# Optimization experiments

Measured on AMD Instinct MI355X. Metric: run time of the kernel, lower is better.

Reference implementation:

```python
import jax, jax.numpy as jnp
import numpy as np

B, S, D, H = 2, 2048, 1024, 16
DK = D // H


def setup_inputs() -> dict:
    key = jax.random.key(0)
    ks = jax.random.split(key, 12)
    scale = 1.0 / np.sqrt(D)
    inp = {
        "pre_Q": jax.random.normal(ks[0], (B, S, D), jnp.float32),
        "pre_K": jax.random.normal(ks[1], (B, S, D), jnp.float32),
        "pre_V": jax.random.normal(ks[2], (B, S, D), jnp.float32),
        "Wq": jax.random.normal(ks[3], (D, D), jnp.float32) * scale,
        "bq": jnp.zeros((D,), jnp.float32),
        "Wk": jax.random.normal(ks[4], (D, D), jnp.float32) * scale,
        "bk": jnp.zeros((D,), jnp.float32),
        "Wv": jax.random.normal(ks[5], (D, D), jnp.float32) * scale,
        "bv": jnp.zeros((D,), jnp.float32),
        "Wo": jax.random.normal(ks[6], (D, D), jnp.float32) * scale,
        "bo": jnp.zeros((D,), jnp.float32),
        "mask": jnp.ones((B, 1, 1, S), jnp.int32),
    }
    return inp


def _split_heads(x):
    # (B, S, D) -> (B, H, S, DK)
    return x.reshape(B, S, H, DK).transpose(0, 2, 1, 3)


def reference(pre_Q, pre_K, pre_V, Wq, bq, Wk, bk, Wv, bv, Wo, bo, mask):
    # linear projections (torch nn.Linear: x @ W.T + b)
    Q = _split_heads(pre_Q @ Wq.T + bq)
    K = _split_heads(pre_K @ Wk.T + bk)
    V = _split_heads(pre_V @ Wv.T + bv)
    # scaled dot-product attention; dropout is identity in eval mode
    scores = jnp.einsum("bhqd,bhkd->bhqk", Q, K) / np.sqrt(DK).astype(np.float32)
    scores = jnp.where(mask == 0, jnp.float32(-1e9), scores)
    weights = jax.nn.softmax(scores, axis=-1)
    ctx = jnp.einsum("bhqk,bhkd->bhqd", weights, V)  # (B, H, S, DK)
    concat = ctx.transpose(0, 2, 1, 3).reshape(B, S, D)
    return concat @ Wo.T + bo
```

## Files before the change

### kernel.cpp

```cpp
#include <hip/hip_runtime.h>

#define SS 2048
#define DD 1024
#define HH 16
#define MM 4096
#define KK 1024

typedef __attribute__((ext_vector_type(8))) short bf16x8;
typedef __attribute__((ext_vector_type(4))) float f32x4;
typedef __attribute__((ext_vector_type(4))) float float4_t;
typedef __attribute__((ext_vector_type(4))) short short4_t;
typedef __attribute__((ext_vector_type(4))) int iv4;

__device__ __forceinline__ short f2bf(float f) {
    union { float f; unsigned u; } x; x.f = f;
    unsigned r = x.u + 0x7fffu + ((x.u >> 16) & 1u);
    return (short)(r >> 16);
}

__device__ __forceinline__ f32x4 mfma16(bf16x8 a, bf16x8 b, f32x4 c) {
    return __builtin_amdgcn_mfma_f32_16x16x32_bf16(a, b, c, 0, 0, 0);
}

__device__ __forceinline__ void gl_lds16(const void* g, void* l) {
    __builtin_amdgcn_global_load_lds(
        (const __attribute__((address_space(1))) void*)g,
        (__attribute__((address_space(3))) void*)l, 16, 0, 0);
}

__global__ __launch_bounds__(256)
void convX(const float* __restrict__ x0, const float* __restrict__ x1,
           const float* __restrict__ x2, short* __restrict__ dst) {
    const float* s = (blockIdx.y == 0) ? x0 : (blockIdx.y == 1) ? x1 : x2;
    const size_t i = ((size_t)blockIdx.x * 256 + threadIdx.x) * 8;
    float4_t a = *(const float4_t*)(s + i);
    float4_t b = *(const float4_t*)(s + i + 4);
    bf16x8 o;
#pragma unroll
    for (int e = 0; e < 4; ++e) { o[e] = f2bf(a[e]); o[4 + e] = f2bf(b[e]); }
    *(bf16x8*)(dst + (size_t)blockIdx.y * MM * KK + i) = o;
}

__global__ __launch_bounds__(256)
void convW(const float* __restrict__ w0, const float* __restrict__ w1,
           const float* __restrict__ w2, const float* __restrict__ w3,
           short* __restrict__ dst) {
    const float* s = (blockIdx.y == 0) ? w0 : (blockIdx.y == 1) ? w1
                   : (blockIdx.y == 2) ? w2 : w3;
    const size_t i = ((size_t)blockIdx.x * 256 + threadIdx.x) * 8;
    float4_t a = *(const float4_t*)(s + i);
    float4_t b = *(const float4_t*)(s + i + 4);
    bf16x8 o;
#pragma unroll
    for (int e = 0; e < 4; ++e) { o[e] = f2bf(a[e]); o[4 + e] = f2bf(b[e]); }
    *(bf16x8*)(dst + (size_t)blockIdx.y * KK * KK + i) = o;
}

__device__ __forceinline__ void gemm_loop(const short* __restrict__ A,
                                          const short* __restrict__ Bw,
                                          int m0, int n0,
                                          short* As, short* Bs,
                                          f32x4 acc[4][4]) {
    const int tid = threadIdx.x;
    const int lane = tid & 63, w = tid >> 6;
    const int wr = w >> 1, wc = w & 1;
    const int lr = lane & 15, lg = lane >> 4;

    const int c1 = tid + 256;
    const int r0 = tid >> 2, o0 = (tid & 3) * 8;
    const int r1 = c1 >> 2, o1 = (c1 & 3) * 8;
    const short* ga0 = A + (size_t)(m0 + r0) * KK + o0;
    const short* ga1 = A + (size_t)(m0 + r1) * KK + o1;
    const short* gb0 = Bw + (size_t)(n0 + r0) * KK + o0;
    const short* gb1 = Bw + (size_t)(n0 + r1) * KK + o1;
    char* lA = (char*)As + tid * 16;
    char* lB = (char*)Bs + tid * 16;

#define GSTAGE(buf, kofs)                                  \
    { gl_lds16(ga0 + (kofs), lA + (buf) * 8192);           \
      gl_lds16(ga1 + (kofs), lA + 4096 + (buf) * 8192);    \
      gl_lds16(gb0 + (kofs), lB + (buf) * 8192);           \
      gl_lds16(gb1 + (kofs), lB + 4096 + (buf) * 8192); }

    GSTAGE(0, 0);
    __syncthreads();
    int cur = 0;
    for (int kt = 0; kt < KK / 32; ++kt) {
        if (kt + 1 < KK / 32) GSTAGE(cur ^ 1, (kt + 1) * 32);
        const char* ba = (const char*)As + cur * 8192;
        const char* bb = (const char*)Bs + cur * 8192;
        bf16x8 af[4], bfr[4];
#pragma unroll
        for (int i = 0; i < 4; ++i) {
            af[i]  = *(const bf16x8*)(ba + (wr * 64 + i * 16 + lr) * 64 + lg * 16);
            bfr[i] = *(const bf16x8*)(bb + (wc * 64 + i * 16 + lr) * 64 + lg * 16);
        }
#pragma unroll
        for (int mi = 0; mi < 4; ++mi)
#pragma unroll
            for (int ni = 0; ni < 4; ++ni)
                acc[mi][ni] = mfma16(af[mi], bfr[ni], acc[mi][ni]);
        __syncthreads();
        cur ^= 1;
    }
#undef GSTAGE
}

__global__ __launch_bounds__(256, 2)
void qkv_gemm(const short* __restrict__ Xb, const short* __restrict__ Wb,
              const float* __restrict__ bq, const float* __restrict__ bk,
              const float* __restrict__ bv,
              short* __restrict__ Qo, short* __restrict__ Ko, short* __restrict__ Vto) {
    __shared__ __align__(16) short As[2 * 4096];
    __shared__ __align__(16) short Bs[2 * 4096];
    const int z = blockIdx.z;
    const short* A = Xb + (size_t)z * MM * KK;
    const short* W = Wb + (size_t)z * KK * KK;
    const float* bias = (z == 0) ? bq : (z == 1) ? bk : bv;
    const float scale = (z == 0) ? 0.125f : 1.0f;
    const int m0 = blockIdx.x * 128, n0 = blockIdx.y * 128;

    f32x4 zero = {0.f, 0.f, 0.f, 0.f};
    f32x4 acc[4][4];
#pragma unroll
    for (int i = 0; i < 4; ++i)
#pragma unroll
        for (int j = 0; j < 4; ++j) acc[i][j] = zero;

    gemm_loop(A, W, m0, n0, As, Bs, acc);

    const int tid = threadIdx.x;
    const int lane = tid & 63, w = tid >> 6;
    const int wr = w >> 1, wc = w & 1;
    const int lr = lane & 15, lg = lane >> 4;

#pragma unroll
    for (int mi = 0; mi < 4; ++mi) {
        const int mbase = m0 + wr * 64 + mi * 16 + lg * 4;
        const int b = mbase >> 11, s = mbase & 2047;
#pragma unroll
        for (int ni = 0; ni < 4; ++ni) {
            const int n = n0 + wc * 64 + ni * 16 + lr;
            const float bvv = bias[n];
            const int h = n >> 6, dk = n & 63;
            if (z == 2) {
                short4_t pk;
#pragma unroll
                for (int r = 0; r < 4; ++r) pk[r] = f2bf(acc[mi][ni][r] + bvv);
                const int sp = (s & ~31) | (lg * 8 + (mi & 1) * 4);
                *(short4_t*)(Vto + ((size_t)((b * HH + h) * 64 + dk) << 11) + sp) = pk;
            } else {
                short* dst = (z == 0) ? Qo : Ko;
#pragma unroll
                for (int r = 0; r < 4; ++r)
                    dst[((size_t)((b * HH + h) * SS + (s + r)) << 6) + dk] =
                        f2bf((acc[mi][ni][r] + bvv) * scale);
            }
        }
    }
}

__global__ __launch_bounds__(256, 2)
void out_gemm(const short* __restrict__ ctx, const short* __restrict__ Wo,
              const float* __restrict__ bo, float* __restrict__ out) {
    __shared__ __align__(16) short As[2 * 4096];
    __shared__ __align__(16) short Bs[2 * 4096];
    const int m0 = blockIdx.x * 128, n0 = blockIdx.y * 128;

    f32x4 zero = {0.f, 0.f, 0.f, 0.f};
    f32x4 acc[4][4];
#pragma unroll
    for (int i = 0; i < 4; ++i)
#pragma unroll
        for (int j = 0; j < 4; ++j) acc[i][j] = zero;

    gemm_loop(ctx, Wo, m0, n0, As, Bs, acc);

    const int tid = threadIdx.x;
    const int lane = tid & 63, w = tid >> 6;
    const int wr = w >> 1, wc = w & 1;
    const int lr = lane & 15, lg = lane >> 4;

#pragma unroll
    for (int mi = 0; mi < 4; ++mi)
#pragma unroll
        for (int ni = 0; ni < 4; ++ni) {
            const int n = n0 + wc * 64 + ni * 16 + lr;
            const float bvv = bo[n];
#pragma unroll
            for (int r = 0; r < 4; ++r) {
                const int m = m0 + wr * 64 + mi * 16 + lg * 4 + r;
                out[(size_t)m * KK + n] = acc[mi][ni][r] + bvv;
            }
        }
}

__global__ __launch_bounds__(256, 2)
void attn_kernel(const short* __restrict__ Qg, const short* __restrict__ Kg,
                 const short* __restrict__ Vtg, const int* __restrict__ mask,
                 short* __restrict__ ctxb) {
    __shared__ __align__(16) short Ks[2][4096];
    __shared__ __align__(16) short Vs[2][4096];

    const int tid = threadIdx.x, w = tid >> 6, lane = tid & 63;
    const int lr = lane & 15, lg = lane >> 4;
    const int bh = blockIdx.y, b = bh >> 4, h = bh & 15;
    const int q0w = blockIdx.x * 64 + w * 16;

    const short* Qh = Qg + (size_t)bh * SS * 64;
    const short* Kh = Kg + (size_t)bh * SS * 64;
    const short* Vh = Vtg + (size_t)bh * 64 * SS;
    const int* mrow = mask + b * SS;

    bf16x8 qf0 = *(const bf16x8*)(Qh + (q0w + lr) * 64 + lg * 8);
    bf16x8 qf1 = *(const bf16x8*)(Qh + (q0w + lr) * 64 + 32 + lg * 8);

    f32x4 zero = {0.f, 0.f, 0.f, 0.f};
    f32x4 octx[4];
#pragma unroll
    for (int dt = 0; dt < 4; ++dt) octx[dt] = zero;
    float mrun = -1e30f, lrun = 0.f;

    const int c1 = tid + 256;
    const int kr0 = tid >> 3, kc0 = ((tid & 7) ^ (kr0 & 7)) * 8;
    const int kr1 = c1 >> 3, kc1 = ((c1 & 7) ^ (kr1 & 7)) * 8;
    const short* gk0 = Kh + kr0 * 64 + kc0;
    const short* gk1 = Kh + kr1 * 64 + kc1;
    const short* gv0 = Vh + (size_t)kr0 * SS + kc0;
    const short* gv1 = Vh + (size_t)kr1 * SS + kc1;
    char* lK = (char*)Ks + tid * 16;
    char* lV = (char*)Vs + tid * 16;

#define ASTAGE(buf, key0)                                    \
    { gl_lds16(gk0 + (key0) * 64, lK + (buf) * 8192);        \
      gl_lds16(gk1 + (key0) * 64, lK + 4096 + (buf) * 8192); \
      gl_lds16(gv0 + (key0), lV + (buf) * 8192);             \
      gl_lds16(gv1 + (key0), lV + 4096 + (buf) * 8192); }

    ASTAGE(0, 0);
    __syncthreads();
    int cur = 0;

    for (int it = 0; it < SS / 64; ++it) {
        const int key0 = it * 64;
        if (it + 1 < SS / 64) ASTAGE(cur ^ 1, key0 + 64);

        const char* bK = (const char*)Ks + cur * 8192;
        const char* bV = (const char*)Vs + cur * 8192;

        f32x4 sc[4];
#pragma unroll
        for (int kb = 0; kb < 4; ++kb) {
            const int row = kb * 16 + lr;
            const char* rb = bK + row * 128;
            const int sw = row & 7;
            bf16x8 k0 = *(const bf16x8*)(rb + ((lg ^ sw) * 16));
            bf16x8 k1 = *(const bf16x8*)(rb + (((4 + lg) ^ sw) * 16));
            f32x4 s = zero;
            s = mfma16(k0, qf0, s);
            s = mfma16(k1, qf1, s);
            sc[kb] = s;
        }
#pragma unroll
        for (int kb = 0; kb < 4; ++kb) {
            iv4 mv = *(const iv4*)(mrow + key0 + kb * 16 + lg * 4);
#pragma unroll
            for (int r = 0; r < 4; ++r)
                if (mv[r] == 0) sc[kb][r] = -1e9f;
        }
        float tm = -1e30f;
#pragma unroll
        for (int kb = 0; kb < 4; ++kb)
#pragma unroll
            for (int r = 0; r < 4; ++r) tm = fmaxf(tm, sc[kb][r]);
        tm = fmaxf(tm, __shfl_xor(tm, 16));
        tm = fmaxf(tm, __shfl_xor(tm, 32));
        const float mnew = fmaxf(mrun, tm);
        float rs = 0.f;
#pragma unroll
        for (int kb = 0; kb < 4; ++kb)
#pragma unroll
            for (int r = 0; r < 4; ++r) {
                const float p = __expf(sc[kb][r] - mnew);
                sc[kb][r] = p;
                rs += p;
            }
        rs += __shfl_xor(rs, 16);
        rs += __shfl_xor(rs, 32);
        const float alpha = __expf(mrun - mnew);
        lrun = lrun * alpha + rs;
        mrun = mnew;

        float aq[4];
#pragma unroll
        for (int r = 0; r < 4; ++r) aq[r] = __shfl(alpha, lg * 4 + r);
#pragma unroll
        for (int dt = 0; dt < 4; ++dt)
#pragma unroll
            for (int r = 0; r < 4; ++r) octx[dt][r] *= aq[r];

        bf16x8 pa01, pa23;
#pragma unroll
        for (int j = 0; j < 4; ++j) {
            pa01[j] = f2bf(sc[0][j]); pa01[4 + j] = f2bf(sc[1][j]);
            pa23[j] = f2bf(sc[2][j]); pa23[4 + j] = f2bf(sc[3][j]);
        }
#pragma unroll
        for (int dt = 0; dt < 4; ++dt) {
            const int row = dt * 16 + lr;
            const char* rb = bV + row * 128;
            const int sw = row & 7;
            bf16x8 v0 = *(const bf16x8*)(rb + ((lg ^ sw) * 16));
            bf16x8 v1 = *(const bf16x8*)(rb + (((4 + lg) ^ sw) * 16));
            octx[dt] = mfma16(pa01, v0, octx[dt]);
            octx[dt] = mfma16(pa23, v1, octx[dt]);
        }
        __syncthreads();
        cur ^= 1;
    }
#undef ASTAGE

    float li[4];
#pragma unroll
    for (int r = 0; r < 4; ++r) li[r] = 1.f / __shfl(lrun, lg * 4 + r);
#pragma unroll
    for (int dt = 0; dt < 4; ++dt)
#pragma unroll
        for (int r = 0; r < 4; ++r)
            ctxb[(size_t)(b * SS + q0w + lg * 4 + r) * DD + h * 64 + dt * 16 + lr] =
                f2bf(octx[dt][r] * li[r]);
}

extern "C" void kernel_launch(void* const* d_in, const int* in_sizes, int n_in,
                              void* d_out, int out_size, void* d_ws, size_t ws_size,
                              hipStream_t stream) {
    const float* preQ = (const float*)d_in[0];
    const float* preK = (const float*)d_in[1];
    const float* preV = (const float*)d_in[2];
    const float* Wq   = (const float*)d_in[3];
    const float* bq   = (const float*)d_in[4];
    const float* Wk   = (const float*)d_in[5];
    const float* bk   = (const float*)d_in[6];
    const float* Wv   = (const float*)d_in[7];
    const float* bv   = (const float*)d_in[8];
    const float* Wo   = (const float*)d_in[9];
    const float* bo   = (const float*)d_in[10];
    const int*   mask = (const int*)d_in[11];
    float* out = (float*)d_out;

    char* ws = (char*)d_ws;
    short* Xb  = (short*)(ws);
    short* Wb  = (short*)(ws + (size_t)25165824);
    short* Qw  = (short*)(ws + (size_t)33554432);
    short* Kw  = (short*)(ws + (size_t)41943040);
    short* Vtw = (short*)(ws + (size_t)50331648);
    short* Ctx = (short*)(ws + (size_t)58720256);

    convX<<<dim3(2048, 3), 256, 0, stream>>>(preQ, preK, preV, Xb);
    convW<<<dim3(512, 4), 256, 0, stream>>>(Wq, Wk, Wv, Wo, Wb);
    qkv_gemm<<<dim3(32, 8, 3), 256, 0, stream>>>(Xb, Wb, bq, bk, bv, Qw, Kw, Vtw);
    attn_kernel<<<dim3(32, 32), 256, 0, stream>>>(Qw, Kw, Vtw, mask, Ctx);
    out_gemm<<<dim3(32, 8), 256, 0, stream>>>(Ctx, Wb + (size_t)3 * KK * KK, bo, out);
}
```

Before: 256.4 us.

## Rewrite attention with 32x32 MFMA tiles, exp2 softmax and lazy rescaling

The attention kernel moves from 16x16x32 to 32x32x16 bf16 MFMA, so each wave handles 32 query rows and each block 128. K and V are loaded into LDS in the MFMA operand layout instead of the XOR swizzle. Softmax now uses exp2, with log2(e) folded into the Q scale, plus a hardware v_exp. The running-max rescale is skipped unless the max grows by more than 8, masking is skipped when the whole mask tile is nonzero, and P is packed with cvt_pk_bf16 and permlane32_swap. Each block now does more work, so the grid halves, which may reduce occupancy and adds register pressure from the larger accumulators.

```diff
diff --git a/kernel.cpp b/kernel.cpp
--- a/kernel.cpp
+++ b/kernel.cpp
@@ -8,9 +8,9 @@
 
 typedef __attribute__((ext_vector_type(8))) short bf16x8;
 typedef __attribute__((ext_vector_type(4))) float f32x4;
+typedef __attribute__((ext_vector_type(16))) float f32x16;
 typedef __attribute__((ext_vector_type(4))) float float4_t;
 typedef __attribute__((ext_vector_type(4))) short short4_t;
-typedef __attribute__((ext_vector_type(4))) int iv4;
 
 __device__ __forceinline__ short f2bf(float f) {
     union { float f; unsigned u; } x; x.f = f;
@@ -21,11 +21,24 @@
 __device__ __forceinline__ f32x4 mfma16(bf16x8 a, bf16x8 b, f32x4 c) {
     return __builtin_amdgcn_mfma_f32_16x16x32_bf16(a, b, c, 0, 0, 0);
 }
+__device__ __forceinline__ f32x16 mfma32(bf16x8 a, bf16x8 b, f32x16 c) {
+    return __builtin_amdgcn_mfma_f32_32x32x16_bf16(a, b, c, 0, 0, 0);
+}
 
 __device__ __forceinline__ void gl_lds16(const void* g, void* l) {
     __builtin_amdgcn_global_load_lds(
         (const __attribute__((address_space(1))) void*)g,
         (__attribute__((address_space(3))) void*)l, 16, 0, 0);
+}
+
+__device__ __forceinline__ float exp2a(float x) {
+    float r; asm("v_exp_f32 %0, %1" : "=v"(r) : "v"(x)); return r;
+}
+__device__ __forceinline__ int cvtpk(float lo, float hi) {
+    int r; asm("v_cvt_pk_bf16_f32 %0, %1, %2" : "=v"(r) : "v"(lo), "v"(hi)); return r;
+}
+__device__ __forceinline__ void pswap(int& a, int& b) {
+    asm("v_permlane32_swap_b32 %0, %1" : "+v"(a), "+v"(b));
 }
 
 __global__ __launch_bounds__(256)
@@ -117,7 +130,7 @@
     const short* A = Xb + (size_t)z * MM * KK;
     const short* W = Wb + (size_t)z * KK * KK;
     const float* bias = (z == 0) ? bq : (z == 1) ? bk : bv;
-    const float scale = (z == 0) ? 0.125f : 1.0f;
+    const float scale = (z == 0) ? 0.125f * 1.44269504088896f : 1.0f;
     const int m0 = blockIdx.x * 128, n0 = blockIdx.y * 128;
 
     f32x4 zero = {0.f, 0.f, 0.f, 0.f};
@@ -147,8 +160,7 @@
                 short4_t pk;
 #pragma unroll
                 for (int r = 0; r < 4; ++r) pk[r] = f2bf(acc[mi][ni][r] + bvv);
-                const int sp = (s & ~31) | (lg * 8 + (mi & 1) * 4);
-                *(short4_t*)(Vto + ((size_t)((b * HH + h) * 64 + dk) << 11) + sp) = pk;
+                *(short4_t*)(Vto + ((size_t)((b * HH + h) * 64 + dk) << 11) + s) = pk;
             } else {
                 short* dst = (z == 0) ? Qo : Ko;
 #pragma unroll
@@ -203,38 +215,37 @@
     __shared__ __align__(16) short Vs[2][4096];
 
     const int tid = threadIdx.x, w = tid >> 6, lane = tid & 63;
-    const int lr = lane & 15, lg = lane >> 4;
+    const int l31 = lane & 31, hi = lane >> 5;
     const int bh = blockIdx.y, b = bh >> 4, h = bh & 15;
-    const int q0w = blockIdx.x * 64 + w * 16;
+    const int q0w = blockIdx.x * 128 + w * 32;
 
     const short* Qh = Qg + (size_t)bh * SS * 64;
     const short* Kh = Kg + (size_t)bh * SS * 64;
     const short* Vh = Vtg + (size_t)bh * 64 * SS;
     const int* mrow = mask + b * SS;
 
-    bf16x8 qf0 = *(const bf16x8*)(Qh + (q0w + lr) * 64 + lg * 8);
-    bf16x8 qf1 = *(const bf16x8*)(Qh + (q0w + lr) * 64 + 32 + lg * 8);
-
-    f32x4 zero = {0.f, 0.f, 0.f, 0.f};
-    f32x4 octx[4];
-#pragma unroll
-    for (int dt = 0; dt < 4; ++dt) octx[dt] = zero;
+    bf16x8 qf[4];
+#pragma unroll
+    for (int t = 0; t < 4; ++t)
+        qf[t] = *(const bf16x8*)(Qh + (q0w + l31) * 64 + t * 16 + hi * 8);
+
+    f32x16 octx0, octx1;
+#pragma unroll
+    for (int r = 0; r < 16; ++r) { octx0[r] = 0.f; octx1[r] = 0.f; }
     float mrun = -1e30f, lrun = 0.f;
 
-    const int c1 = tid + 256;
-    const int kr0 = tid >> 3, kc0 = ((tid & 7) ^ (kr0 & 7)) * 8;
-    const int kr1 = c1 >> 3, kc1 = ((c1 & 7) ^ (kr1 & 7)) * 8;
-    const short* gk0 = Kh + kr0 * 64 + kc0;
-    const short* gk1 = Kh + kr1 * 64 + kc1;
-    const short* gv0 = Vh + (size_t)kr0 * SS + kc0;
-    const short* gv1 = Vh + (size_t)kr1 * SS + kc1;
+    const int tq = (tid >> 6) & 3;
+    const short* gk0 = Kh + (l31) * 64 + tq * 16 + hi * 8;
+    const short* gk1 = Kh + (32 + l31) * 64 + tq * 16 + hi * 8;
+    const short* gv0 = Vh + (size_t)(l31) * SS + tq * 16 + hi * 8;
+    const short* gv1 = Vh + (size_t)(32 + l31) * SS + tq * 16 + hi * 8;
     char* lK = (char*)Ks + tid * 16;
     char* lV = (char*)Vs + tid * 16;
 
-#define ASTAGE(buf, key0)                                    \
-    { gl_lds16(gk0 + (key0) * 64, lK + (buf) * 8192);        \
-      gl_lds16(gk1 + (key0) * 64, lK + 4096 + (buf) * 8192); \
-      gl_lds16(gv0 + (key0), lV + (buf) * 8192);             \
+#define ASTAGE(buf, key0)                                      \
+    { gl_lds16(gk0 + (key0) * 64, lK + (buf) * 8192);          \
+      gl_lds16(gk1 + (key0) * 64, lK + 4096 + (buf) * 8192);   \
+      gl_lds16(gv0 + (key0), lV + (buf) * 8192);               \
       gl_lds16(gv1 + (key0), lV + 4096 + (buf) * 8192); }
 
     ASTAGE(0, 0);
@@ -245,90 +256,113 @@
         const int key0 = it * 64;
         if (it + 1 < SS / 64) ASTAGE(cur ^ 1, key0 + 64);
 
-        const char* bK = (const char*)Ks + cur * 8192;
-        const char* bV = (const char*)Vs + cur * 8192;
-
-        f32x4 sc[4];
-#pragma unroll
-        for (int kb = 0; kb < 4; ++kb) {
-            const int row = kb * 16 + lr;
-            const char* rb = bK + row * 128;
-            const int sw = row & 7;
-            bf16x8 k0 = *(const bf16x8*)(rb + ((lg ^ sw) * 16));
-            bf16x8 k1 = *(const bf16x8*)(rb + (((4 + lg) ^ sw) * 16));
-            f32x4 s = zero;
-            s = mfma16(k0, qf0, s);
-            s = mfma16(k1, qf1, s);
-            sc[kb] = s;
-        }
-#pragma unroll
-        for (int kb = 0; kb < 4; ++kb) {
-            iv4 mv = *(const iv4*)(mrow + key0 + kb * 16 + lg * 4);
-#pragma unroll
-            for (int r = 0; r < 4; ++r)
-                if (mv[r] == 0) sc[kb][r] = -1e9f;
-        }
-        float tm = -1e30f;
-#pragma unroll
-        for (int kb = 0; kb < 4; ++kb)
-#pragma unroll
-            for (int r = 0; r < 4; ++r) tm = fmaxf(tm, sc[kb][r]);
-        tm = fmaxf(tm, __shfl_xor(tm, 16));
+        const char* cK = (const char*)Ks + cur * 8192;
+        const char* cV = (const char*)Vs + cur * 8192;
+
+        f32x16 s0, s1;
+#pragma unroll
+        for (int r = 0; r < 16; ++r) { s0[r] = 0.f; s1[r] = 0.f; }
+#pragma unroll
+        for (int t = 0; t < 4; ++t) {
+            bf16x8 a0 = *(const bf16x8*)(cK + ((0 * 4 + t) * 64 + lane) * 16);
+            bf16x8 a1 = *(const bf16x8*)(cK + ((1 * 4 + t) * 64 + lane) * 16);
+            s0 = mfma32(a0, qf[t], s0);
+            s1 = mfma32(a1, qf[t], s1);
+        }
+
+        const int mk = mrow[key0 + lane];
+        if (!__all(mk != 0)) {
+#pragma unroll
+            for (int r = 0; r < 16; ++r) {
+                const int kl = (r & 3) + 8 * (r >> 2) + 4 * hi;
+                if (mrow[key0 + kl] == 0) s0[r] = -1e9f;
+                if (mrow[key0 + 32 + kl] == 0) s1[r] = -1e9f;
+            }
+        }
+
+        float tv[16];
+#pragma unroll
+        for (int r = 0; r < 16; ++r) tv[r] = fmaxf(s0[r], s1[r]);
+#pragma unroll
+        for (int off = 8; off >= 1; off >>= 1)
+#pragma unroll
+            for (int r = 0; r < 8; ++r)
+                if (r < off) tv[r] = fmaxf(tv[r], tv[r + off]);
+        float tm = tv[0];
         tm = fmaxf(tm, __shfl_xor(tm, 32));
-        const float mnew = fmaxf(mrun, tm);
-        float rs = 0.f;
-#pragma unroll
-        for (int kb = 0; kb < 4; ++kb)
-#pragma unroll
-            for (int r = 0; r < 4; ++r) {
-                const float p = __expf(sc[kb][r] - mnew);
-                sc[kb][r] = p;
-                rs += p;
-            }
-        rs += __shfl_xor(rs, 16);
+
+        if (!__all(tm <= mrun + 8.0f)) {
+            const float mnew = fmaxf(mrun, tm);
+            const float alpha = exp2a(mrun - mnew);
+            lrun *= alpha;
+#pragma unroll
+            for (int r = 0; r < 16; ++r) {
+                const int ql = (r & 3) + 8 * (r >> 2) + 4 * hi;
+                const float aq = __shfl(alpha, ql);
+                octx0[r] *= aq;
+                octx1[r] *= aq;
+            }
+            mrun = mnew;
+        }
+
+#pragma unroll
+        for (int r = 0; r < 16; ++r) {
+            s0[r] = exp2a(s0[r] - mrun);
+            s1[r] = exp2a(s1[r] - mrun);
+        }
+        float sv[16];
+#pragma unroll
+        for (int r = 0; r < 16; ++r) sv[r] = s0[r] + s1[r];
+#pragma unroll
+        for (int off = 8; off >= 1; off >>= 1)
+#pragma unroll
+            for (int r = 0; r < 8; ++r)
+                if (r < off) sv[r] += sv[r + off];
+        float rs = sv[0];
         rs += __shfl_xor(rs, 32);
-        const float alpha = __expf(mrun - mnew);
-        lrun = lrun * alpha + rs;
-        mrun = mnew;
-
-        float aq[4];
-#pragma unroll
-        for (int r = 0; r < 4; ++r) aq[r] = __shfl(alpha, lg * 4 + r);
-#pragma unroll
-        for (int dt = 0; dt < 4; ++dt)
-#pragma unroll
-            for (int r = 0; r < 4; ++r) octx[dt][r] *= aq[r];
-
-        bf16x8 pa01, pa23;
-#pragma unroll
-        for (int j = 0; j < 4; ++j) {
-            pa01[j] = f2bf(sc[0][j]); pa01[4 + j] = f2bf(sc[1][j]);
-            pa23[j] = f2bf(sc[2][j]); pa23[4 + j] = f2bf(sc[3][j]);
-        }
-#pragma unroll
-        for (int dt = 0; dt < 4; ++dt) {
-            const int row = dt * 16 + lr;
-            const char* rb = bV + row * 128;
-            const int sw = row & 7;
-            bf16x8 v0 = *(const bf16x8*)(rb + ((lg ^ sw) * 16));
-            bf16x8 v1 = *(const bf16x8*)(rb + (((4 + lg) ^ sw) * 16));
-            octx[dt] = mfma16(pa01, v0, octx[dt]);
-            octx[dt] = mfma16(pa23, v1, octx[dt]);
-        }
+        lrun += rs;
+
+        bf16x8 pa[4];
+#pragma unroll
+        for (int kb = 0; kb < 2; ++kb) {
+            const f32x16& sv16 = kb ? s1 : s0;
+#pragma unroll
+            for (int half = 0; half < 2; ++half) {
+                const int base = half * 8;
+                int A  = cvtpk(sv16[base + 0], sv16[base + 1]);
+                int Bw = cvtpk(sv16[base + 2], sv16[base + 3]);
+                int Cw = cvtpk(sv16[base + 4], sv16[base + 5]);
+                int Dw = cvtpk(sv16[base + 6], sv16[base + 7]);
+                pswap(A, Cw);
+                pswap(Bw, Dw);
+                union { int wv[4]; bf16x8 v; } u;
+                u.wv[0] = A; u.wv[1] = Bw; u.wv[2] = Cw; u.wv[3] = Dw;
+                pa[kb * 2 + half] = u.v;
+            }
+        }
+
+#pragma unroll
+        for (int kk = 0; kk < 4; ++kk) {
+            bf16x8 v0 = *(const bf16x8*)(cV + ((0 * 4 + kk) * 64 + lane) * 16);
+            bf16x8 v1 = *(const bf16x8*)(cV + ((1 * 4 + kk) * 64 + lane) * 16);
+            octx0 = mfma32(pa[kk], v0, octx0);
+            octx1 = mfma32(pa[kk], v1, octx1);
+        }
+
         __syncthreads();
         cur ^= 1;
     }
 #undef ASTAGE
 
-    float li[4];
-#pragma unroll
-    for (int r = 0; r < 4; ++r) li[r] = 1.f / __shfl(lrun, lg * 4 + r);
-#pragma unroll
-    for (int dt = 0; dt < 4; ++dt)
-#pragma unroll
-        for (int r = 0; r < 4; ++r)
-            ctxb[(size_t)(b * SS + q0w + lg * 4 + r) * DD + h * 64 + dt * 16 + lr] =
-                f2bf(octx[dt][r] * li[r]);
+    const float linv = 1.f / lrun;
+#pragma unroll
+    for (int r = 0; r < 16; ++r) {
+        const int ql = (r & 3) + 8 * (r >> 2) + 4 * hi;
+        const float li = __shfl(linv, ql);
+        short* orow = ctxb + (size_t)(b * SS + q0w + ql) * DD + h * 64 + l31;
+        orow[0]  = f2bf(octx0[r] * li);
+        orow[32] = f2bf(octx1[r] * li);
+    }
 }
 
 extern "C" void kernel_launch(void* const* d_in, const int* in_sizes, int n_in,
@@ -359,6 +393,6 @@
     convX<<<dim3(2048, 3), 256, 0, stream>>>(preQ, preK, preV, Xb);
     convW<<<dim3(512, 4), 256, 0, stream>>>(Wq, Wk, Wv, Wo, Wb);
     qkv_gemm<<<dim3(32, 8, 3), 256, 0, stream>>>(Xb, Wb, bq, bk, bv, Qw, Kw, Vtw);
-    attn_kernel<<<dim3(32, 32), 256, 0, stream>>>(Qw, Kw, Vtw, mask, Ctx);
+    attn_kernel<<<dim3(16, 32), 256, 0, stream>>>(Qw, Kw, Vtw, mask, Ctx);
     out_gemm<<<dim3(32, 8), 256, 0, stream>>>(Ctx, Wb + (size_t)3 * KK * KK, bo, out);
 }
```

Measured after the change: 240.5 us. 6.2% less time.
